# Kernel optimization log

Hardware: AMD Instinct MI355X
Metric: run time of the kernel (lower is better)

The kernel has to match this reference:

```python
import jax, jax.numpy as jnp
import numpy as np

D = 64
N = 262144


def _stack_four(A, B, C, Dm):
    return jnp.block([[A, B], [C, Dm]])


def setup_inputs() -> dict:
    key = jax.random.key(0)
    # Z: (2d+1, n+1) in-context prompt matrix
    Z = jax.random.normal(key, (2 * D + 1, N + 1), dtype=jnp.float32)
    # P: zeros with P[-1,-1] = 1 (selects last row)
    P = jnp.zeros((2 * D + 1, 2 * D + 1), dtype=jnp.float32).at[-1, -1].set(1.0)
    # Q: block matrix built from M1, M2, B as in TFLayer.__init__
    I = jnp.eye(D, dtype=jnp.float32)
    O = jnp.zeros((D, D), dtype=jnp.float32)
    M1 = _stack_four(-I, I, O, O)
    M2 = -M1
    Bm = _stack_four(I, O, O, O)  # C = eye(d), so C.T = I
    A = M2.T @ Bm @ M1            # (2d, 2d)
    Q = jnp.zeros((2 * D + 1, 2 * D + 1), dtype=jnp.float32).at[: 2 * D, : 2 * D].set(A)
    return {"Z": Z, "P": P, "Q": Q}


def reference(Z, P, Q):
    # next_Z = Z + (1/n) * P @ Z @ M @ Z.T @ Q @ Z
    # M = eye(n+1) with M[-1,-1] = 0, i.e. right-mult by M zeroes the last
    # column. We never materialize the (n+1, n+1) identity.
    n = Z.shape[1] - 1
    PZ = P @ Z                         # (2d+1, n+1)
    PZM = PZ.at[:, -1].set(0.0)        # apply M: zero last column
    S = PZM @ Z.T                      # (2d+1, 2d+1) -- the only big contraction
    upd = (S @ Q) @ Z                  # (2d+1, n+1)
    return Z + upd / n
```

## Files before the change

kernel.cpp:

```cpp
#include <hip/hip_runtime.h>

#define ROWS    129
#define NCOLS   262145
#define NDOT    262144
#define DOTROWS 128
#define CHUNK   16384
#define NCHUNK  16

__global__ void k_dot(const float* __restrict__ Z, float* __restrict__ partials) {
    const int row   = blockIdx.x & (DOTROWS - 1);
    const int chunk = blockIdx.x >> 7;
    const long base = (long)chunk * CHUNK;
    const float* zr = Z + (long)row * NCOLS + base;
    const float* zl = Z + (long)DOTROWS * NCOLS + base;
    const int tid = threadIdx.x;

    float acc = 0.f;
#pragma unroll 8
    for (int k = 0; k < CHUNK / 256; ++k) {
        const int c = tid + k * 256;
        acc = fmaf(zr[c], zl[c], acc);
    }
#pragma unroll
    for (int off = 32; off; off >>= 1) acc += __shfl_down(acc, off, 64);
    __shared__ float s[4];
    if ((tid & 63) == 0) s[tid >> 6] = acc;
    __syncthreads();
    if (tid == 0) {
        partials[chunk * DOTROWS + row] = s[0] + s[1] + s[2] + s[3];
    }
}

__global__ void k_t(const float* __restrict__ partials,
                    const float* __restrict__ Q,
                    float* __restrict__ t) {
    __shared__ float v[DOTROWS];
    const int tid = threadIdx.x;
    float s = 0.f;
#pragma unroll
    for (int c = 0; c < NCHUNK; ++c) s += partials[c * DOTROWS + tid];
    v[tid] = s;
    __syncthreads();
    float acc = 0.f;
#pragma unroll 8
    for (int m = 0; m < DOTROWS; ++m) acc = fmaf(v[m], Q[m * ROWS + tid], acc);
    t[tid] = acc * (1.0f / (float)NDOT);
}

__global__ void k_update(const float* __restrict__ Z,
                         const float* __restrict__ t,
                         float* __restrict__ out) {
    __shared__ float ts[DOTROWS];
    const int tid = threadIdx.x;
    if (tid < DOTROWS) ts[tid] = t[tid];
    __syncthreads();

    const long c = (long)blockIdx.x * blockDim.x + tid;
    if (c >= NCOLS) return;

    float acc = 0.f;
#pragma unroll 8
    for (int j = 0; j < DOTROWS; ++j) {
        const float val = Z[(long)j * NCOLS + c];
        out[(long)j * NCOLS + c] = val;
        acc = fmaf(ts[j], val, acc);
    }
    const float zl = Z[(long)DOTROWS * NCOLS + c];
    out[(long)DOTROWS * NCOLS + c] = zl + acc;
}

extern "C" void kernel_launch(void* const* d_in, const int* in_sizes, int n_in,
                              void* d_out, int out_size, void* d_ws, size_t ws_size,
                              hipStream_t stream) {
    const float* Z = (const float*)d_in[0];
    const float* Q = (const float*)d_in[2];
    float* out = (float*)d_out;

    float* partials = (float*)d_ws;
    float* t        = partials + NCHUNK * DOTROWS;

    k_dot<<<NCHUNK * DOTROWS, 256, 0, stream>>>(Z, partials);
    k_t<<<1, DOTROWS, 0, stream>>>(partials, Q, t);
    k_update<<<(NCOLS + 255) / 256, 256, 0, stream>>>(Z, t, out);
}
```

Before: 281.1 us.

## Move row copy into dot kernel and fold t computation into update kernel

The copy of rows 0..127 to the output now happens in the dot-product pass, which already reads those rows, so the update pass only writes the last row. The small kernel that reduces partials and multiplies by Q is folded into the update kernel, with every block recomputing the 128-element t vector redundantly. This removes one launch and one full re-read-and-write of the first 128 rows in the update pass. The update pass still reads all rows of Z, and each of roughly a thousand blocks now performs a 128x128 matvec on top of that.

```diff
diff --git a/kernel.cpp b/kernel.cpp
--- a/kernel.cpp
+++ b/kernel.cpp
@@ -7,19 +7,23 @@
 #define CHUNK   16384
 #define NCHUNK  16
 
-__global__ void k_dot(const float* __restrict__ Z, float* __restrict__ partials) {
+__global__ void k_dot_copy(const float* __restrict__ Z, float* __restrict__ out,
+                           float* __restrict__ partials) {
     const int row   = blockIdx.x & (DOTROWS - 1);
     const int chunk = blockIdx.x >> 7;
     const long base = (long)chunk * CHUNK;
     const float* zr = Z + (long)row * NCOLS + base;
     const float* zl = Z + (long)DOTROWS * NCOLS + base;
+    float*       po = out + (long)row * NCOLS + base;
     const int tid = threadIdx.x;
 
     float acc = 0.f;
 #pragma unroll 8
     for (int k = 0; k < CHUNK / 256; ++k) {
         const int c = tid + k * 256;
-        acc = fmaf(zr[c], zl[c], acc);
+        const float zv = zr[c];
+        po[c] = zv;
+        acc = fmaf(zv, zl[c], acc);
     }
 #pragma unroll
     for (int off = 32; off; off >>= 1) acc += __shfl_down(acc, off, 64);
@@ -29,30 +33,31 @@
     if (tid == 0) {
         partials[chunk * DOTROWS + row] = s[0] + s[1] + s[2] + s[3];
     }
+    if (blockIdx.x == 0 && tid < DOTROWS) {
+        out[(long)tid * NCOLS + NDOT] = Z[(long)tid * NCOLS + NDOT];
+    }
 }
 
-__global__ void k_t(const float* __restrict__ partials,
-                    const float* __restrict__ Q,
-                    float* __restrict__ t) {
+__global__ void k_finish(const float* __restrict__ Z,
+                         const float* __restrict__ partials,
+                         const float* __restrict__ Q,
+                         float* __restrict__ out) {
     __shared__ float v[DOTROWS];
-    const int tid = threadIdx.x;
-    float s = 0.f;
-#pragma unroll
-    for (int c = 0; c < NCHUNK; ++c) s += partials[c * DOTROWS + tid];
-    v[tid] = s;
-    __syncthreads();
-    float acc = 0.f;
-#pragma unroll 8
-    for (int m = 0; m < DOTROWS; ++m) acc = fmaf(v[m], Q[m * ROWS + tid], acc);
-    t[tid] = acc * (1.0f / (float)NDOT);
-}
-
-__global__ void k_update(const float* __restrict__ Z,
-                         const float* __restrict__ t,
-                         float* __restrict__ out) {
     __shared__ float ts[DOTROWS];
     const int tid = threadIdx.x;
-    if (tid < DOTROWS) ts[tid] = t[tid];
+    if (tid < DOTROWS) {
+        float s = 0.f;
+#pragma unroll
+        for (int c = 0; c < NCHUNK; ++c) s += partials[c * DOTROWS + tid];
+        v[tid] = s;
+    }
+    __syncthreads();
+    if (tid < DOTROWS) {
+        float acc = 0.f;
+#pragma unroll 8
+        for (int m = 0; m < DOTROWS; ++m) acc = fmaf(v[m], Q[m * ROWS + tid], acc);
+        ts[tid] = acc * (1.0f / (float)NDOT);
+    }
     __syncthreads();
 
     const long c = (long)blockIdx.x * blockDim.x + tid;
@@ -61,12 +66,9 @@
     float acc = 0.f;
 #pragma unroll 8
     for (int j = 0; j < DOTROWS; ++j) {
-        const float val = Z[(long)j * NCOLS + c];
-        out[(long)j * NCOLS + c] = val;
-        acc = fmaf(ts[j], val, acc);
+        acc = fmaf(ts[j], Z[(long)j * NCOLS + c], acc);
     }
-    const float zl = Z[(long)DOTROWS * NCOLS + c];
-    out[(long)DOTROWS * NCOLS + c] = zl + acc;
+    out[(long)DOTROWS * NCOLS + c] = Z[(long)DOTROWS * NCOLS + c] + acc;
 }
 
 extern "C" void kernel_launch(void* const* d_in, const int* in_sizes, int n_in,
@@ -77,9 +79,7 @@
     float* out = (float*)d_out;
 
     float* partials = (float*)d_ws;
-    float* t        = partials + NCHUNK * DOTROWS;
 
-    k_dot<<<NCHUNK * DOTROWS, 256, 0, stream>>>(Z, partials);
-    k_t<<<1, DOTROWS, 0, stream>>>(partials, Q, t);
-    k_update<<<(NCOLS + 255) / 256, 256, 0, stream>>>(Z, t, out);
+    k_dot_copy<<<NCHUNK * DOTROWS, 256, 0, stream>>>(Z, out, partials);
+    k_finish<<<(NCOLS + 255) / 256, 256, 0, stream>>>(Z, partials, Q, out);
 }
```

Result: no change. 282.1 us (+0.3%).
